# Kernel tuning notes

Hardware: AMD Instinct MI355X
Metric: run time of the kernel (lower is better)

The kernel has to match this reference:

```python
import jax, jax.numpy as jnp
import numpy as np

M = 8      # num_modules
H = 128    # hidden_size per module
IN = 512   # input_size
MH = M * H

def _block_mask():
    # mask[mi*H:(mi+1)*H, mi*H:] = 1 (module mi reads modules >= mi)
    m = np.zeros((MH, MH), dtype=np.float32)
    for mi in range(M):
        m[mi*H:(mi+1)*H, mi*H:] = 1.0
    return jnp.asarray(m)

def _active_sizes(T):
    # number of active modules at step t: t=0 -> M, else min(M, trailing_zeros(t)+1)
    sizes = []
    for t in range(T):
        ma = 0
        while t % (2 ** ma) == 0 and ma < M:
            ma += 1
        sizes.append(ma * H)
    return jnp.asarray(np.array(sizes, dtype=np.int32))

def setup_inputs() -> dict:
    key = jax.random.key(0)
    k1, k2, k3, k4 = jax.random.split(key, 4)
    T, B = 256, 128
    scale = 1.0 / np.sqrt(MH)
    x = jax.random.normal(k1, (T, B, IN), dtype=jnp.float32)
    h_prev = jnp.zeros((B, MH), dtype=jnp.float32)
    Wxh = jax.random.normal(k2, (MH, IN), dtype=jnp.float32) * scale
    Whh = jax.random.normal(k3, (MH, MH), dtype=jnp.float32) * scale
    bh = jax.random.normal(k4, (MH,), dtype=jnp.float32) * scale
    return {"x": x, "h_prev": h_prev, "Wxh": Wxh, "Whh": Whh, "bh": bh}

def reference(x, h_prev, Wxh, Whh, bh):
    T = x.shape[0]
    mask = _block_mask()
    Whh_m = Whh * mask  # clockwork block-triangular mask, reapplied as in torch
    thresholds = _active_sizes(T)          # [T] active hidden width per step
    idx = jnp.arange(MH)

    # Precompute input projections for all timesteps: [T, B, MH]
    xW = jnp.einsum('tbi,hi->tbh', x, Wxh)

    def step(h, inp):
        xw_t, thr = inp
        # full-width update; rows < thr equal the torch sliced-matmul result
        h_full = h @ Whh_m.T + xw_t + bh
        h_new = jnp.where(idx < thr, h_full, h)
        return h_new, h_new

    h_last, out = jax.lax.scan(step, h_prev, (xW, thresholds))
    return (out, h_last)
```

## Files before the change

kernel.cpp:

```cpp
#include <hip/hip_runtime.h>
#include <hip/hip_bf16.h>


#define TT 256
#define BB 128
#define INW 512
#define HH 128
#define MHW 1024

typedef __bf16 bf16x8 __attribute__((ext_vector_type(8)));
typedef __bf16 bf16x4 __attribute__((ext_vector_type(4)));
typedef float f32x4 __attribute__((ext_vector_type(4)));

__constant__ unsigned int c_hmod_off[8] = {
    0u, 4194304u, 6291456u, 7340032u, 7864320u, 8126464u, 8257536u, 8323072u};

__device__ __forceinline__ int active_thr(int t) {
    int ma = (t == 0) ? 8 : min(__ffs(t), 8);
    return ma * HH;
}

__device__ __forceinline__ unsigned short f2bf(float f) {
    union { float f; unsigned int u; } v{f};
    unsigned int r = v.u + 0x7FFFu + ((v.u >> 16) & 1u);
    return (unsigned short)(r >> 16);
}
__device__ __forceinline__ unsigned int pack2(float lo, float hi) {
    return (unsigned int)f2bf(lo) | ((unsigned int)f2bf(hi) << 16);
}
__device__ __forceinline__ float bf2f(unsigned short u) {
    union { unsigned int i; float f; } v;
    v.i = ((unsigned int)u) << 16;
    return v.f;
}

__device__ __forceinline__ void gld_lds16(const float* g, char* l) {
    __builtin_amdgcn_global_load_lds(
        (const __attribute__((address_space(1))) void*)g,
        (__attribute__((address_space(3))) void*)l, 16, 0, 0);
}

#define TILE_B 16384

__device__ __forceinline__ void stage_load(float4 (&v)[8],
                                           const float* __restrict__ src,
                                           int stride, int tid) {
    int k4 = (tid & 15) * 4;
    int r0 = tid >> 4;
#pragma unroll
    for (int p = 0; p < 8; ++p)
        v[p] = *reinterpret_cast<const float4*>(src + (size_t)(p * 16 + r0) * stride + k4);
}

__device__ __forceinline__ void stage_write(char* dst, const float4 (&v)[8], int tid) {
    int k8 = (tid & 15) * 8;
    int r0 = tid >> 4;
#pragma unroll
    for (int p = 0; p < 8; ++p) {
        int row = p * 16 + r0;
        ushort4 b;
        b.x = f2bf(v[p].x); b.y = f2bf(v[p].y);
        b.z = f2bf(v[p].z); b.w = f2bf(v[p].w);
        int off = (row * 128 + k8) ^ ((row & 7) << 4);
        *reinterpret_cast<ushort4*>(dst + off) = b;
    }
}

__device__ __forceinline__ void stage_load_h16(uint4 (&v)[4],
                                               const unsigned short* __restrict__ src,
                                               int tid) {
    int k16 = (tid & 7) * 8;
    int r0 = tid >> 3;
#pragma unroll
    for (int p = 0; p < 4; ++p)
        v[p] = *reinterpret_cast<const uint4*>(src + (size_t)(p * 32 + r0) * HH + k16);
}
__device__ __forceinline__ void stage_write_h16(char* dst, const uint4 (&v)[4], int tid) {
    int k16 = (tid & 7) * 8;
    int r0 = tid >> 3;
#pragma unroll
    for (int p = 0; p < 4; ++p) {
        int row = p * 32 + r0;
        int off = (row * 128 + k16 * 2) ^ ((row & 7) << 4);
        *reinterpret_cast<uint4*>(dst + off) = v[p];
    }
}

__device__ __forceinline__ bf16x8 frag_ld(const char* tile, int row, int ks, int lane) {
    int off = (row * 128 + ks * 64 + (lane >> 4) * 16) ^ ((row & 7) << 4);
    return *reinterpret_cast<const bf16x8*>(tile + off);
}

__device__ __forceinline__ bf16x8 frag_ld_f32(const char* tile, int row, int ks, int g) {
    int off = ((row << 8) + ks * 128 + g * 32) ^ ((row & 7) << 4);
    f32x4 a = *reinterpret_cast<const f32x4*>(tile + off);
    f32x4 b = *reinterpret_cast<const f32x4*>(tile + (off ^ 16));
    bf16x8 u;
    u[0] = (__bf16)a[0]; u[1] = (__bf16)a[1]; u[2] = (__bf16)a[2]; u[3] = (__bf16)a[3];
    u[4] = (__bf16)b[0]; u[5] = (__bf16)b[1]; u[6] = (__bf16)b[2]; u[7] = (__bf16)b[3];
    return u;
}

__device__ __forceinline__ void mfma_tile(const char* sA, const char* sB,
                                          f32x4 (&acc)[4][4], int lane,
                                          int wr, int wc) {
#pragma unroll
    for (int ks = 0; ks < 2; ++ks) {
        bf16x8 fa[4], fb[4];
#pragma unroll
        for (int i = 0; i < 4; ++i) {
            fa[i] = frag_ld(sA, wr + i * 16 + (lane & 15), ks, lane);
            fb[i] = frag_ld(sB, wc + i * 16 + (lane & 15), ks, lane);
        }
#pragma unroll
        for (int i = 0; i < 4; ++i)
#pragma unroll
            for (int j = 0; j < 4; ++j)
                acc[i][j] = __builtin_amdgcn_mfma_f32_16x16x32_bf16(
                    fa[i], fb[j], acc[i][j], 0, 0, 0);
    }
}

__global__ __launch_bounds__(256) void k_xw(const float* __restrict__ x,
                                            const float* __restrict__ Wxh,
                                            const float* __restrict__ bh,
                                            float* __restrict__ xwb) {
    __shared__ char ldsW[2][32768];
    __shared__ char ldsX[2][16384];
    int id = blockIdx.x >> 1, half = blockIdx.x & 1;
    int rt = 0, rem = id;
    while (rem >= (256 >> rt)) { rem -= 256 >> rt; ++rt; }
    int t = rem << rt;

    int tid = threadIdx.x, lane = tid & 63, wid = tid >> 6;
    int l15 = lane & 15, g = lane >> 4;
    int wr = (wid >> 1) * 64, wc = (wid & 1) * 32;

    const float* gW[8];
    const float* gX[4];
    {
        int kb = (lane & 15) * 16;
#pragma unroll
        for (int i = 0; i < 8; ++i) {
            int row = i * 16 + wid * 4 + (lane >> 4);
            int kf = (kb ^ ((row & 7) << 4)) >> 2;
            gW[i] = Wxh + (size_t)(rt * 128 + row) * INW + kf;
        }
#pragma unroll
        for (int i = 0; i < 4; ++i) {
            int row = i * 16 + wid * 4 + (lane >> 4);
            int kf = (kb ^ ((row & 7) << 4)) >> 2;
            gX[i] = x + ((size_t)t * BB + half * 64 + row) * INW + kf;
        }
    }
#pragma unroll
    for (int i = 0; i < 8; ++i)
        gld_lds16(gW[i], &ldsW[0][0] + i * 4096 + wid * 1024);
#pragma unroll
    for (int i = 0; i < 4; ++i)
        gld_lds16(gX[i], &ldsX[0][0] + i * 4096 + wid * 1024);

    f32x4 acc[4][2] = {};
    for (int c = 0; c < 8; ++c) {
        int cur = c & 1;
        __syncthreads();
        if (c < 7) {
#pragma unroll
            for (int i = 0; i < 8; ++i)
                gld_lds16(gW[i] + (c + 1) * 64,
                          &ldsW[cur ^ 1][0] + i * 4096 + wid * 1024);
#pragma unroll
            for (int i = 0; i < 4; ++i)
                gld_lds16(gX[i] + (c + 1) * 64,
                          &ldsX[cur ^ 1][0] + i * 4096 + wid * 1024);
        }
#pragma unroll
        for (int ks = 0; ks < 2; ++ks) {
            bf16x8 fa[4], fb[2];
#pragma unroll
            for (int i = 0; i < 4; ++i)
                fa[i] = frag_ld_f32(&ldsW[cur][0], wr + i * 16 + l15, ks, g);
#pragma unroll
            for (int j = 0; j < 2; ++j)
                fb[j] = frag_ld_f32(&ldsX[cur][0], wc + j * 16 + l15, ks, g);
#pragma unroll
            for (int i = 0; i < 4; ++i)
#pragma unroll
                for (int j = 0; j < 2; ++j)
                    acc[i][j] = __builtin_amdgcn_mfma_f32_16x16x32_bf16(
                        fa[i], fb[j], acc[i][j], 0, 0, 0);
        }
    }
#pragma unroll
    for (int i = 0; i < 4; ++i) {
        int rbase = rt * 128 + wr + i * 16 + g * 4;
        float4 bias = *reinterpret_cast<const float4*>(&bh[rbase]);
#pragma unroll
        for (int j = 0; j < 2; ++j) {
            int b = half * 64 + wc + j * 16 + l15;
            float4 v = make_float4(acc[i][j][0] + bias.x, acc[i][j][1] + bias.y,
                                   acc[i][j][2] + bias.z, acc[i][j][3] + bias.w);
            *reinterpret_cast<float4*>(
                &xwb[(size_t)(t * BB + b) * MHW + rbase]) = v;
        }
    }
}

__global__ __launch_bounds__(256) void k_u(const float* __restrict__ Whh,
                                           const float* __restrict__ hprev,
                                           const unsigned short* __restrict__ hmod,
                                           float* __restrict__ xwb, int mi) {
    int k = blockIdx.x;
    int t = k << mi;
    __shared__ char lds[4 * TILE_B];
    int tid = threadIdx.x, lane = tid & 63, wid = tid >> 6;
    int wr = (wid >> 1) * 64, wc = (wid & 1) * 64;

    int ntile = 2 * (7 - mi);
    f32x4 acc[4][4] = {};

    if (k == 0) {
        auto srcs = [&](int tt, const float*& pa, const float*& ph) {
            int j = mi + 1 + (tt >> 1);
            int c0 = (tt & 1) * 64;
            pa = Whh + (size_t)(mi * HH) * MHW + j * HH + c0;
            ph = hprev + j * HH + c0;
        };
        float4 vA[8], vH[8];
        const float *pa, *ph;
        srcs(0, pa, ph);
        stage_load(vA, pa, MHW, tid);
        stage_load(vH, ph, MHW, tid);
        stage_write(lds, vA, tid);
        stage_write(lds + TILE_B, vH, tid);
        for (int tt = 0; tt < ntile; ++tt) {
            int cur = tt & 1;
            __syncthreads();
            if (tt + 1 < ntile) {
                srcs(tt + 1, pa, ph);
                stage_load(vA, pa, MHW, tid);
                stage_load(vH, ph, MHW, tid);
            }
            mfma_tile(lds + cur * 2 * TILE_B, lds + cur * 2 * TILE_B + TILE_B,
                      acc, lane, wr, wc);
            if (tt + 1 < ntile) {
                stage_write(lds + (cur ^ 1) * 2 * TILE_B, vA, tid);
                stage_write(lds + (cur ^ 1) * 2 * TILE_B + TILE_B, vH, tid);
            }
        }
    } else {
        auto srcs = [&](int tt, const float*& pa, const unsigned short*& ph) {
            int j = mi + 1 + (tt >> 1);
            int c0 = (tt & 1) * 64;
            pa = Whh + (size_t)(mi * HH) * MHW + j * HH + c0;
            int g = (t - 1) >> j;
            ph = hmod + c_hmod_off[j] + (size_t)g * BB * HH + c0;
        };
        float4 vA[8];
        uint4 vH[4];
        const float* pa;
        const unsigned short* ph;
        srcs(0, pa, ph);
        stage_load(vA, pa, MHW, tid);
        stage_load_h16(vH, ph, tid);
        stage_write(lds, vA, tid);
        stage_write_h16(lds + TILE_B, vH, tid);
        for (int tt = 0; tt < ntile; ++tt) {
            int cur = tt & 1;
            __syncthreads();
            if (tt + 1 < ntile) {
                srcs(tt + 1, pa, ph);
                stage_load(vA, pa, MHW, tid);
                stage_load_h16(vH, ph, tid);
            }
            mfma_tile(lds + cur * 2 * TILE_B, lds + cur * 2 * TILE_B + TILE_B,
                      acc, lane, wr, wc);
            if (tt + 1 < ntile) {
                stage_write(lds + (cur ^ 1) * 2 * TILE_B, vA, tid);
                stage_write_h16(lds + (cur ^ 1) * 2 * TILE_B + TILE_B, vH, tid);
            }
        }
    }
#pragma unroll
    for (int i = 0; i < 4; ++i) {
        int rbase = wr + i * 16 + (lane >> 4) * 4;
#pragma unroll
        for (int j = 0; j < 4; ++j) {
            int b = wc + j * 16 + (lane & 15);
            float4* p = reinterpret_cast<float4*>(
                &xwb[(size_t)(t * BB + b) * MHW + mi * HH + rbase]);
            float4 v = *p;
            v.x += acc[i][j][0]; v.y += acc[i][j][1];
            v.z += acc[i][j][2]; v.w += acc[i][j][3];
            *p = v;
        }
    }
}

#define SYNC_LDS()                                              \
    do {                                                        \
        asm volatile("s_waitcnt lgkmcnt(0)" ::: "memory");      \
        __builtin_amdgcn_sched_barrier(0);                      \
        __builtin_amdgcn_s_barrier();                           \
        __builtin_amdgcn_sched_barrier(0);                      \
    } while (0)
#define SYNC_VM24()                                             \
    do {                                                        \
        asm volatile("s_waitcnt vmcnt(24)" ::: "memory");       \
        __builtin_amdgcn_sched_barrier(0);                      \
        __builtin_amdgcn_s_barrier();                           \
        __builtin_amdgcn_sched_barrier(0);                      \
    } while (0)

__global__ __launch_bounds__(256) void k_phase(const float* __restrict__ Whh,
                                               const float* __restrict__ hprev,
                                               const float* __restrict__ xwb,
                                               unsigned short* __restrict__ hmod,
                                               int mi) {
    int b0 = blockIdx.x * 16;
    int tid = threadIdx.x, lane = tid & 63, wid = tid >> 6;
    int l15 = lane & 15, g = lane >> 4;
    __shared__ char sH[2][4096];
    __shared__ char sU[8][8192];
    int Tm = TT >> mi;

    if (wid < 2) {
        bf16x8 Af[4][4];
        {
            const float* Ab = Whh + (size_t)(mi * HH) * MHW + mi * HH;
#pragma unroll
            for (int mm = 0; mm < 4; ++mm) {
                const float* row = Ab + (size_t)(64 * wid + mm * 16 + l15) * MHW;
#pragma unroll
                for (int kf = 0; kf < 4; ++kf) {
                    float4 v0 = *reinterpret_cast<const float4*>(row + kf * 32 + g * 8);
                    float4 v1 = *reinterpret_cast<const float4*>(row + kf * 32 + g * 8 + 4);
                    bf16x8 u;
                    u[0] = (__bf16)v0.x; u[1] = (__bf16)v0.y;
                    u[2] = (__bf16)v0.z; u[3] = (__bf16)v0.w;
                    u[4] = (__bf16)v1.x; u[5] = (__bf16)v1.y;
                    u[6] = (__bf16)v1.z; u[7] = (__bf16)v1.w;
                    Af[mm][kf] = u;
                }
            }
        }
#pragma unroll
        for (int p = 0; p < 2; ++p) {
            int tt = tid + p * 128;
            int b = tt >> 4, r8 = (tt & 15) * 8;
            const float* hp = hprev + (size_t)(b0 + b) * MHW + mi * HH + r8;
            float4 v0 = *reinterpret_cast<const float4*>(hp);
            float4 v1 = *reinterpret_cast<const float4*>(hp + 4);
            uint4 pk;
            pk.x = pack2(v0.x, v0.y); pk.y = pack2(v0.z, v0.w);
            pk.z = pack2(v1.x, v1.y); pk.w = pack2(v1.z, v1.w);
            int off = (b * 256 + r8 * 2) ^ ((b & 7) << 4);
            *reinterpret_cast<uint4*>(&sH[0][0] + off) = pk;
        }
        int roff[4], woff[4], uoff[4];
#pragma unroll
        for (int kf = 0; kf < 4; ++kf)
            roff[kf] = (l15 * 256 + kf * 64 + g * 16) ^ ((l15 & 7) << 4);
#pragma unroll
        for (int mm = 0; mm < 4; ++mm) {
            woff[mm] = (l15 * 256 + (64 * wid + mm * 16 + g * 4) * 2) ^ ((l15 & 7) << 4);
            uoff[mm] = (16 * wid + 4 * mm + g) * 256 + l15 * 16;
        }
        SYNC_LDS();

        for (int K = 0; K < Tm; ++K) {
            int cur = K & 1;
            const char* ub = &sU[K & 7][0];
            f32x4 acc[4], acc2[4];
#pragma unroll
            for (int mm = 0; mm < 4; ++mm) {
                acc[mm] = *reinterpret_cast<const f32x4*>(ub + uoff[mm]);
                acc2[mm] = (f32x4){0.f, 0.f, 0.f, 0.f};
            }
            bf16x8 Bf[4];
#pragma unroll
            for (int kf = 0; kf < 4; ++kf)
                Bf[kf] = *reinterpret_cast<const bf16x8*>(&sH[cur][0] + roff[kf]);
#pragma unroll
            for (int mm = 0; mm < 4; ++mm) {
                acc[mm] = __builtin_amdgcn_mfma_f32_16x16x32_bf16(
                    Af[mm][0], Bf[0], acc[mm], 0, 0, 0);
                acc2[mm] = __builtin_amdgcn_mfma_f32_16x16x32_bf16(
                    Af[mm][2], Bf[2], acc2[mm], 0, 0, 0);
                acc[mm] = __builtin_amdgcn_mfma_f32_16x16x32_bf16(
                    Af[mm][1], Bf[1], acc[mm], 0, 0, 0);
                acc2[mm] = __builtin_amdgcn_mfma_f32_16x16x32_bf16(
                    Af[mm][3], Bf[3], acc2[mm], 0, 0, 0);
            }
#pragma unroll
            for (int mm = 0; mm < 4; ++mm) {
                acc[mm] += acc2[mm];
                bf16x4 pk;
                pk[0] = (__bf16)acc[mm][0]; pk[1] = (__bf16)acc[mm][1];
                pk[2] = (__bf16)acc[mm][2]; pk[3] = (__bf16)acc[mm][3];
                *reinterpret_cast<bf16x4*>(&sH[cur ^ 1][0] + woff[mm]) = pk;
            }
            SYNC_LDS();
        }
    } else if (wid == 2) {
        const float* ubase = xwb + (size_t)(b0 + l15) * MHW + mi * HH + g * 4;
#pragma unroll
        for (int q = 0; q < 4; ++q) {
            int t = min(q, Tm - 1) << mi;
            const float* pt = ubase + (size_t)t * BB * MHW;
#pragma unroll
            for (int p = 0; p < 8; ++p)
                gld_lds16(pt + p * 16, &sU[q][0] + p * 1024);
        }
        SYNC_VM24();
        for (int K = 0; K < Tm; ++K) {
            int t = min(K + 4, Tm - 1) << mi;
            int slot = (K + 4) & 7;
            const float* pt = ubase + (size_t)t * BB * MHW;
#pragma unroll
            for (int p = 0; p < 8; ++p)
                gld_lds16(pt + p * 16, &sU[slot][0] + p * 1024);
            SYNC_VM24();
        }
        asm volatile("s_waitcnt vmcnt(0)" ::: "memory");
    } else {
        int bq = lane >> 2;
        int rr = (lane & 3) * 32;
        unsigned short* hm =
            hmod + c_hmod_off[mi] + (size_t)(b0 + bq) * HH + rr;
        int soff[4];
#pragma unroll
        for (int c = 0; c < 4; ++c)
            soff[c] = (bq * 256 + (rr + c * 8) * 2) ^ ((bq & 7) << 4);
        SYNC_LDS();
        for (int K = 0; K < Tm; ++K) {
            if (K >= 1) {
                uint4 h[4];
#pragma unroll
                for (int c = 0; c < 4; ++c)
                    h[c] = *reinterpret_cast<const uint4*>(&sH[K & 1][0] + soff[c]);
                unsigned short* dst = hm + (size_t)(K - 1) * BB * HH;
#pragma unroll
                for (int c = 0; c < 4; ++c)
                    *reinterpret_cast<uint4*>(dst + c * 8) = h[c];
            }
            SYNC_LDS();
        }
        {
            uint4 h[4];
#pragma unroll
            for (int c = 0; c < 4; ++c)
                h[c] = *reinterpret_cast<const uint4*>(&sH[Tm & 1][0] + soff[c]);
            unsigned short* dst = hm + (size_t)(Tm - 1) * BB * HH;
#pragma unroll
            for (int c = 0; c < 4; ++c)
                *reinterpret_cast<uint4*>(dst + c * 8) = h[c];
        }
    }
}

__global__ __launch_bounds__(256) void k_out(const unsigned short* __restrict__ hmod,
                                             float* __restrict__ out) {
    int b = blockIdx.x, t = blockIdx.y;
    int tid = threadIdx.x;
    int i = tid * 4;
    int j = i >> 7;
    int k = t >> j;
    ushort4 h = *reinterpret_cast<const ushort4*>(
        &hmod[c_hmod_off[j] + ((size_t)k * BB + b) * HH + (i & 127)]);
    float4 v = make_float4(bf2f(h.x), bf2f(h.y), bf2f(h.z), bf2f(h.w));
    *reinterpret_cast<float4*>(&out[((size_t)t * BB + b) * MHW + i]) = v;
    if (t == TT - 1) {
        *reinterpret_cast<float4*>(
            &out[(size_t)TT * BB * MHW + (size_t)b * MHW + i]) = v;
    }
}

extern "C" void kernel_launch(void* const* d_in, const int* in_sizes, int n_in,
                              void* d_out, int out_size, void* d_ws, size_t ws_size,
                              hipStream_t stream) {
    const float* x = (const float*)d_in[0];
    const float* hprev = (const float*)d_in[1];
    const float* Wxh = (const float*)d_in[2];
    const float* Whh = (const float*)d_in[3];
    const float* bh = (const float*)d_in[4];
    float* out = (float*)d_out;

    float* xwb = out;
    unsigned short* hmod = (unsigned short*)d_ws;

    k_xw<<<dim3(1020), 256, 0, stream>>>(x, Wxh, bh, xwb);

    for (int mi = 7; mi >= 0; --mi) {
        if (mi < 7)
            k_u<<<dim3(TT >> mi), 256, 0, stream>>>(Whh, hprev, hmod, xwb, mi);
        k_phase<<<8, 256, 0, stream>>>(Whh, hprev, xwb, hmod, mi);
    }

    k_out<<<dim3(128, 256), 256, 0, stream>>>(hmod, out);
}
```

Baseline: 469.7 us.

## Halve sequential recurrence steps by squaring the diagonal block (A^2 doubling)

Precomputes A^2 for each module's diagonal recurrence block and a combined input term v = A·u_even + u_odd, so the serial phase kernel advances two timesteps per iteration and only produces odd-indexed states. A parallel k_even kernel then fills in the even-indexed states from the preceding odd state. This halves the length of the latency-bound sequential chain, at the cost of two extra parallel kernels per module and extra bf16 rounding through the squared matrix.

```diff
diff --git a/kernel.cpp b/kernel.cpp
--- a/kernel.cpp
+++ b/kernel.cpp
@@ -202,6 +202,52 @@
                                    acc[i][j][2] + bias.z, acc[i][j][3] + bias.w);
             *reinterpret_cast<float4*>(
                 &xwb[(size_t)(t * BB + b) * MHW + rbase]) = v;
+        }
+    }
+}
+
+__global__ __launch_bounds__(256) void k_a2(const float* __restrict__ Whh,
+                                            float* __restrict__ a2) {
+    int mi = blockIdx.x;
+    __shared__ char lds[2 * TILE_B];
+    int tid = threadIdx.x, lane = tid & 63, wid = tid >> 6;
+    int l15 = lane & 15, g = lane >> 4;
+    int wr = (wid >> 1) * 64, wc = (wid & 1) * 64;
+    const float* Ab = Whh + (size_t)(mi * HH) * MHW + mi * HH;
+    f32x4 acc[4][4] = {};
+    for (int c0 = 0; c0 < 128; c0 += 64) {
+        float4 vA[8];
+        stage_load(vA, Ab + c0, MHW, tid);
+        __syncthreads();
+        stage_write(lds, vA, tid);
+        {
+            int k4 = (tid & 15) * 4;
+            int r0 = tid >> 4;
+#pragma unroll
+            for (int p = 0; p < 8; ++p) {
+                int row = p * 16 + r0;
+                ushort4 b;
+                b.x = f2bf(Ab[(size_t)(c0 + k4 + 0) * MHW + row]);
+                b.y = f2bf(Ab[(size_t)(c0 + k4 + 1) * MHW + row]);
+                b.z = f2bf(Ab[(size_t)(c0 + k4 + 2) * MHW + row]);
+                b.w = f2bf(Ab[(size_t)(c0 + k4 + 3) * MHW + row]);
+                int off = (row * 128 + k4 * 2) ^ ((row & 7) << 4);
+                *reinterpret_cast<ushort4*>(lds + TILE_B + off) = b;
+            }
+        }
+        __syncthreads();
+        mfma_tile(lds, lds + TILE_B, acc, lane, wr, wc);
+    }
+    float* dst = a2 + mi * 16384;
+#pragma unroll
+    for (int i = 0; i < 4; ++i) {
+        int r0 = wr + i * 16 + g * 4;
+#pragma unroll
+        for (int jq = 0; jq < 4; ++jq) {
+            int c = wc + jq * 16 + l15;
+#pragma unroll
+            for (int rr = 0; rr < 4; ++rr)
+                dst[(size_t)(r0 + rr) * 128 + c] = acc[i][jq][rr];
         }
     }
 }
@@ -297,6 +343,130 @@
     }
 }
 
+__global__ __launch_bounds__(256) void k_v(const float* __restrict__ Whh,
+                                           const float* __restrict__ xwb,
+                                           float* __restrict__ vbuf, int mi) {
+    int j = blockIdx.x;
+    int t0 = (2 * j) << mi, t1 = (2 * j + 1) << mi;
+    __shared__ char lds[4 * TILE_B];
+    int tid = threadIdx.x, lane = tid & 63, wid = tid >> 6;
+    int l15 = lane & 15, g = lane >> 4;
+    int wr = (wid >> 1) * 64, wc = (wid & 1) * 64;
+
+    const float* Ab = Whh + (size_t)(mi * HH) * MHW + mi * HH;
+    const float* Hb = xwb + (size_t)t0 * BB * MHW + mi * HH;
+    float4 vA[8], vH[8];
+    stage_load(vA, Ab, MHW, tid);
+    stage_load(vH, Hb, MHW, tid);
+    stage_write(lds, vA, tid);
+    stage_write(lds + TILE_B, vH, tid);
+    f32x4 acc[4][4] = {};
+    for (int tt = 0; tt < 2; ++tt) {
+        int cur = tt & 1;
+        __syncthreads();
+        if (tt == 0) {
+            stage_load(vA, Ab + 64, MHW, tid);
+            stage_load(vH, Hb + 64, MHW, tid);
+        }
+        mfma_tile(lds + cur * 2 * TILE_B, lds + cur * 2 * TILE_B + TILE_B,
+                  acc, lane, wr, wc);
+        if (tt == 0) {
+            stage_write(lds + 2 * TILE_B, vA, tid);
+            stage_write(lds + 3 * TILE_B, vH, tid);
+        }
+    }
+#pragma unroll
+    for (int i = 0; i < 4; ++i) {
+        int rbase = wr + i * 16 + g * 4;
+#pragma unroll
+        for (int jq = 0; jq < 4; ++jq) {
+            int b = wc + jq * 16 + l15;
+            float4 u1 = *reinterpret_cast<const float4*>(
+                &xwb[(size_t)(t1 * BB + b) * MHW + mi * HH + rbase]);
+            float4 v = make_float4(acc[i][jq][0] + u1.x, acc[i][jq][1] + u1.y,
+                                   acc[i][jq][2] + u1.z, acc[i][jq][3] + u1.w);
+            *reinterpret_cast<float4*>(
+                &vbuf[((size_t)j * BB + b) * HH + rbase]) = v;
+        }
+    }
+}
+
+__global__ __launch_bounds__(256) void k_even(const float* __restrict__ Whh,
+                                              const float* __restrict__ hprev,
+                                              const float* __restrict__ xwb,
+                                              unsigned short* __restrict__ hmod,
+                                              int mi) {
+    int j = blockIdx.x;
+    int t0 = (2 * j) << mi;
+    __shared__ char lds[4 * TILE_B];
+    int tid = threadIdx.x, lane = tid & 63, wid = tid >> 6;
+    int l15 = lane & 15, g = lane >> 4;
+    int wr = (wid >> 1) * 64, wc = (wid & 1) * 64;
+
+    const float* Ab = Whh + (size_t)(mi * HH) * MHW + mi * HH;
+    f32x4 acc[4][4] = {};
+    if (j == 0) {
+        const float* Hb = hprev + mi * HH;
+        float4 vA[8], vH[8];
+        stage_load(vA, Ab, MHW, tid);
+        stage_load(vH, Hb, MHW, tid);
+        stage_write(lds, vA, tid);
+        stage_write(lds + TILE_B, vH, tid);
+        for (int tt = 0; tt < 2; ++tt) {
+            int cur = tt & 1;
+            __syncthreads();
+            if (tt == 0) {
+                stage_load(vA, Ab + 64, MHW, tid);
+                stage_load(vH, Hb + 64, MHW, tid);
+            }
+            mfma_tile(lds + cur * 2 * TILE_B, lds + cur * 2 * TILE_B + TILE_B,
+                      acc, lane, wr, wc);
+            if (tt == 0) {
+                stage_write(lds + 2 * TILE_B, vA, tid);
+                stage_write(lds + 3 * TILE_B, vH, tid);
+            }
+        }
+    } else {
+        const unsigned short* Hb =
+            hmod + c_hmod_off[mi] + (size_t)(2 * j - 1) * BB * HH;
+        float4 vA[8];
+        uint4 vH[4];
+        stage_load(vA, Ab, MHW, tid);
+        stage_load_h16(vH, Hb, tid);
+        stage_write(lds, vA, tid);
+        stage_write_h16(lds + TILE_B, vH, tid);
+        for (int tt = 0; tt < 2; ++tt) {
+            int cur = tt & 1;
+            __syncthreads();
+            if (tt == 0) {
+                stage_load(vA, Ab + 64, MHW, tid);
+                stage_load_h16(vH, Hb + 64, tid);
+            }
+            mfma_tile(lds + cur * 2 * TILE_B, lds + cur * 2 * TILE_B + TILE_B,
+                      acc, lane, wr, wc);
+            if (tt == 0) {
+                stage_write(lds + 2 * TILE_B, vA, tid);
+                stage_write_h16(lds + 3 * TILE_B, vH, tid);
+            }
+        }
+    }
+#pragma unroll
+    for (int i = 0; i < 4; ++i) {
+        int rbase = wr + i * 16 + g * 4;
+#pragma unroll
+        for (int jq = 0; jq < 4; ++jq) {
+            int b = wc + jq * 16 + l15;
+            float4 u0 = *reinterpret_cast<const float4*>(
+                &xwb[(size_t)(t0 * BB + b) * MHW + mi * HH + rbase]);
+            uint2 pk;
+            pk.x = pack2(acc[i][jq][0] + u0.x, acc[i][jq][1] + u0.y);
+            pk.y = pack2(acc[i][jq][2] + u0.z, acc[i][jq][3] + u0.w);
+            *reinterpret_cast<uint2*>(
+                &hmod[c_hmod_off[mi] + ((size_t)(2 * j) * BB + b) * HH + rbase]) = pk;
+        }
+    }
+}
+
 #define SYNC_LDS()                                              \
     do {                                                        \
         asm volatile("s_waitcnt lgkmcnt(0)" ::: "memory");      \
@@ -312,9 +482,9 @@
         __builtin_amdgcn_sched_barrier(0);                      \
     } while (0)
 
-__global__ __launch_bounds__(256) void k_phase(const float* __restrict__ Whh,
+__global__ __launch_bounds__(256) void k_phase(const float* __restrict__ a2,
                                                const float* __restrict__ hprev,
-                                               const float* __restrict__ xwb,
+                                               const float* __restrict__ vbuf,
                                                unsigned short* __restrict__ hmod,
                                                int mi) {
     int b0 = blockIdx.x * 16;
@@ -322,15 +492,15 @@
     int l15 = lane & 15, g = lane >> 4;
     __shared__ char sH[2][4096];
     __shared__ char sU[8][8192];
-    int Tm = TT >> mi;
+    int Tm_s = 128 >> mi;
 
     if (wid < 2) {
         bf16x8 Af[4][4];
         {
-            const float* Ab = Whh + (size_t)(mi * HH) * MHW + mi * HH;
+            const float* Ab = a2 + mi * 16384;
 #pragma unroll
             for (int mm = 0; mm < 4; ++mm) {
-                const float* row = Ab + (size_t)(64 * wid + mm * 16 + l15) * MHW;
+                const float* row = Ab + (size_t)(64 * wid + mm * 16 + l15) * 128;
 #pragma unroll
                 for (int kf = 0; kf < 4; ++kf) {
                     float4 v0 = *reinterpret_cast<const float4*>(row + kf * 32 + g * 8);
@@ -368,7 +538,7 @@
         }
         SYNC_LDS();
 
-        for (int K = 0; K < Tm; ++K) {
+        for (int K = 0; K < Tm_s; ++K) {
             int cur = K & 1;
             const char* ub = &sU[K & 7][0];
             f32x4 acc[4], acc2[4];
@@ -403,20 +573,20 @@
             SYNC_LDS();
         }
     } else if (wid == 2) {
-        const float* ubase = xwb + (size_t)(b0 + l15) * MHW + mi * HH + g * 4;
+        const float* ubase = vbuf + (size_t)(b0 + l15) * HH + g * 4;
 #pragma unroll
         for (int q = 0; q < 4; ++q) {
-            int t = min(q, Tm - 1) << mi;
-            const float* pt = ubase + (size_t)t * BB * MHW;
+            int jj = min(q, Tm_s - 1);
+            const float* pt = ubase + (size_t)jj * BB * HH;
 #pragma unroll
             for (int p = 0; p < 8; ++p)
                 gld_lds16(pt + p * 16, &sU[q][0] + p * 1024);
         }
         SYNC_VM24();
-        for (int K = 0; K < Tm; ++K) {
-            int t = min(K + 4, Tm - 1) << mi;
+        for (int K = 0; K < Tm_s; ++K) {
+            int jj = min(K + 4, Tm_s - 1);
             int slot = (K + 4) & 7;
-            const float* pt = ubase + (size_t)t * BB * MHW;
+            const float* pt = ubase + (size_t)jj * BB * HH;
 #pragma unroll
             for (int p = 0; p < 8; ++p)
                 gld_lds16(pt + p * 16, &sU[slot][0] + p * 1024);
@@ -433,13 +603,13 @@
         for (int c = 0; c < 4; ++c)
             soff[c] = (bq * 256 + (rr + c * 8) * 2) ^ ((bq & 7) << 4);
         SYNC_LDS();
-        for (int K = 0; K < Tm; ++K) {
+        for (int K = 0; K < Tm_s; ++K) {
             if (K >= 1) {
                 uint4 h[4];
 #pragma unroll
                 for (int c = 0; c < 4; ++c)
                     h[c] = *reinterpret_cast<const uint4*>(&sH[K & 1][0] + soff[c]);
-                unsigned short* dst = hm + (size_t)(K - 1) * BB * HH;
+                unsigned short* dst = hm + (size_t)(2 * K - 1) * BB * HH;
 #pragma unroll
                 for (int c = 0; c < 4; ++c)
                     *reinterpret_cast<uint4*>(dst + c * 8) = h[c];
@@ -450,8 +620,8 @@
             uint4 h[4];
 #pragma unroll
             for (int c = 0; c < 4; ++c)
-                h[c] = *reinterpret_cast<const uint4*>(&sH[Tm & 1][0] + soff[c]);
-            unsigned short* dst = hm + (size_t)(Tm - 1) * BB * HH;
+                h[c] = *reinterpret_cast<const uint4*>(&sH[Tm_s & 1][0] + soff[c]);
+            unsigned short* dst = hm + (size_t)(2 * Tm_s - 1) * BB * HH;
 #pragma unroll
             for (int c = 0; c < 4; ++c)
                 *reinterpret_cast<uint4*>(dst + c * 8) = h[c];
@@ -488,13 +658,18 @@
 
     float* xwb = out;
     unsigned short* hmod = (unsigned short*)d_ws;
+    float* vbuf = (float*)((char*)d_ws + 16711680);
+    float* a2 = (float*)((char*)d_ws + 16711680 + 8388608);
 
     k_xw<<<dim3(1020), 256, 0, stream>>>(x, Wxh, bh, xwb);
+    k_a2<<<dim3(8), 256, 0, stream>>>(Whh, a2);
 
     for (int mi = 7; mi >= 0; --mi) {
         if (mi < 7)
             k_u<<<dim3(TT >> mi), 256, 0, stream>>>(Whh, hprev, hmod, xwb, mi);
-        k_phase<<<8, 256, 0, stream>>>(Whh, hprev, xwb, hmod, mi);
+        k_v<<<dim3(128 >> mi), 256, 0, stream>>>(Whh, xwb, vbuf, mi);
+        k_phase<<<8, 256, 0, stream>>>(a2, hprev, vbuf, hmod, mi);
+        k_even<<<dim3(128 >> mi), 256, 0, stream>>>(Whh, hprev, xwb, hmod, mi);
     }
 
     k_out<<<dim3(128, 256), 256, 0, stream>>>(hmod, out);
```

After: 511.7 us. 1.09x slower.

## Split recurrence into odd/even chains using squared diagonal block A^2

Applied to the files above, without the earlier changes.

Precomputes the squared diagonal recurrence block A^2 per module in a new kernel. The phase kernel then runs two independent half-length chains, odd and even steps, on separate warps, so h_{k+2} = A^2 h_k + A u_{k+1} + u_{k+2}. This roughly halves the serial dependency length of the sequential scan and doubles the warps and U prefetch buffers in flight. In exchange each step does twice the MFMA work, uses more registers and LDS, and adds extra bf16 rounding through A^2 and the converted u fragments.

```diff
diff --git a/kernel.cpp b/kernel.cpp
--- a/kernel.cpp
+++ b/kernel.cpp
@@ -202,6 +202,52 @@
                                    acc[i][j][2] + bias.z, acc[i][j][3] + bias.w);
             *reinterpret_cast<float4*>(
                 &xwb[(size_t)(t * BB + b) * MHW + rbase]) = v;
+        }
+    }
+}
+
+__global__ __launch_bounds__(256) void k_a2(const float* __restrict__ Whh,
+                                            float* __restrict__ a2) {
+    int mi = blockIdx.x;
+    __shared__ char lds[2 * TILE_B];
+    int tid = threadIdx.x, lane = tid & 63, wid = tid >> 6;
+    int l15 = lane & 15, g = lane >> 4;
+    int wr = (wid >> 1) * 64, wc = (wid & 1) * 64;
+    const float* Ab = Whh + (size_t)(mi * HH) * MHW + mi * HH;
+    f32x4 acc[4][4] = {};
+    for (int c0 = 0; c0 < 128; c0 += 64) {
+        float4 vA[8];
+        stage_load(vA, Ab + c0, MHW, tid);
+        __syncthreads();
+        stage_write(lds, vA, tid);
+        {
+            int k4 = (tid & 15) * 4;
+            int r0 = tid >> 4;
+#pragma unroll
+            for (int p = 0; p < 8; ++p) {
+                int row = p * 16 + r0;
+                ushort4 b;
+                b.x = f2bf(Ab[(size_t)(c0 + k4 + 0) * MHW + row]);
+                b.y = f2bf(Ab[(size_t)(c0 + k4 + 1) * MHW + row]);
+                b.z = f2bf(Ab[(size_t)(c0 + k4 + 2) * MHW + row]);
+                b.w = f2bf(Ab[(size_t)(c0 + k4 + 3) * MHW + row]);
+                int off = (row * 128 + k4 * 2) ^ ((row & 7) << 4);
+                *reinterpret_cast<ushort4*>(lds + TILE_B + off) = b;
+            }
+        }
+        __syncthreads();
+        mfma_tile(lds, lds + TILE_B, acc, lane, wr, wc);
+    }
+    float* dst = a2 + mi * 16384;
+#pragma unroll
+    for (int i = 0; i < 4; ++i) {
+        int r0 = wr + i * 16 + g * 4;
+#pragma unroll
+        for (int jq = 0; jq < 4; ++jq) {
+            int c = wc + jq * 16 + l15;
+#pragma unroll
+            for (int rr = 0; rr < 4; ++rr)
+                dst[(size_t)(r0 + rr) * 128 + c] = acc[i][jq][rr];
         }
     }
 }
@@ -304,15 +350,16 @@
         __builtin_amdgcn_s_barrier();                           \
         __builtin_amdgcn_sched_barrier(0);                      \
     } while (0)
-#define SYNC_VM24()                                             \
+#define SYNC_VM(NS)                                             \
     do {                                                        \
-        asm volatile("s_waitcnt vmcnt(24)" ::: "memory");       \
+        asm volatile("s_waitcnt vmcnt(" NS ")" ::: "memory");   \
         __builtin_amdgcn_sched_barrier(0);                      \
         __builtin_amdgcn_s_barrier();                           \
         __builtin_amdgcn_sched_barrier(0);                      \
     } while (0)
 
-__global__ __launch_bounds__(256) void k_phase(const float* __restrict__ Whh,
+__global__ __launch_bounds__(512) void k_phase(const float* __restrict__ a2,
+                                               const float* __restrict__ Whh,
                                                const float* __restrict__ hprev,
                                                const float* __restrict__ xwb,
                                                unsigned short* __restrict__ hmod,
@@ -320,77 +367,160 @@
     int b0 = blockIdx.x * 16;
     int tid = threadIdx.x, lane = tid & 63, wid = tid >> 6;
     int l15 = lane & 15, g = lane >> 4;
-    __shared__ char sH[2][4096];
-    __shared__ char sU[8][8192];
-    int Tm = TT >> mi;
-
-    if (wid < 2) {
-        bf16x8 Af[4][4];
+    __shared__ char sHo[2][4096];
+    __shared__ char sHe[2][4096];
+    __shared__ char sU[16][8192];
+    int Tm = TT >> mi, Tm2 = Tm >> 1;
+
+    if (wid < 4) {
+        int w = wid & 1;
+        bool is_odd = wid < 2;
+        char(*sH)[4096] = is_odd ? sHo : sHe;
+
+        bf16x8 A2f[4][4], A1f[4][4];
         {
-            const float* Ab = Whh + (size_t)(mi * HH) * MHW + mi * HH;
+            const float* Ab2 = a2 + mi * 16384;
+            const float* Ab1 = Whh + (size_t)(mi * HH) * MHW + mi * HH;
 #pragma unroll
             for (int mm = 0; mm < 4; ++mm) {
-                const float* row = Ab + (size_t)(64 * wid + mm * 16 + l15) * MHW;
+                const float* r2 = Ab2 + (size_t)(64 * w + mm * 16 + l15) * 128;
+                const float* r1 = Ab1 + (size_t)(64 * w + mm * 16 + l15) * MHW;
 #pragma unroll
                 for (int kf = 0; kf < 4; ++kf) {
-                    float4 v0 = *reinterpret_cast<const float4*>(row + kf * 32 + g * 8);
-                    float4 v1 = *reinterpret_cast<const float4*>(row + kf * 32 + g * 8 + 4);
-                    bf16x8 u;
-                    u[0] = (__bf16)v0.x; u[1] = (__bf16)v0.y;
-                    u[2] = (__bf16)v0.z; u[3] = (__bf16)v0.w;
-                    u[4] = (__bf16)v1.x; u[5] = (__bf16)v1.y;
-                    u[6] = (__bf16)v1.z; u[7] = (__bf16)v1.w;
-                    Af[mm][kf] = u;
+                    float4 a0 = *reinterpret_cast<const float4*>(r2 + kf * 32 + g * 8);
+                    float4 a1 = *reinterpret_cast<const float4*>(r2 + kf * 32 + g * 8 + 4);
+                    float4 b0v = *reinterpret_cast<const float4*>(r1 + kf * 32 + g * 8);
+                    float4 b1v = *reinterpret_cast<const float4*>(r1 + kf * 32 + g * 8 + 4);
+                    bf16x8 u2, u1;
+                    u2[0] = (__bf16)a0.x; u2[1] = (__bf16)a0.y;
+                    u2[2] = (__bf16)a0.z; u2[3] = (__bf16)a0.w;
+                    u2[4] = (__bf16)a1.x; u2[5] = (__bf16)a1.y;
+                    u2[6] = (__bf16)a1.z; u2[7] = (__bf16)a1.w;
+                    u1[0] = (__bf16)b0v.x; u1[1] = (__bf16)b0v.y;
+                    u1[2] = (__bf16)b0v.z; u1[3] = (__bf16)b0v.w;
+                    u1[4] = (__bf16)b1v.x; u1[5] = (__bf16)b1v.y;
+                    u1[6] = (__bf16)b1v.z; u1[7] = (__bf16)b1v.w;
+                    A2f[mm][kf] = u2;
+                    A1f[mm][kf] = u1;
                 }
             }
         }
-#pragma unroll
-        for (int p = 0; p < 2; ++p) {
-            int tt = tid + p * 128;
-            int b = tt >> 4, r8 = (tt & 15) * 8;
-            const float* hp = hprev + (size_t)(b0 + b) * MHW + mi * HH + r8;
-            float4 v0 = *reinterpret_cast<const float4*>(hp);
-            float4 v1 = *reinterpret_cast<const float4*>(hp + 4);
-            uint4 pk;
-            pk.x = pack2(v0.x, v0.y); pk.y = pack2(v0.z, v0.w);
-            pk.z = pack2(v1.x, v1.y); pk.w = pack2(v1.z, v1.w);
-            int off = (b * 256 + r8 * 2) ^ ((b & 7) << 4);
-            *reinterpret_cast<uint4*>(&sH[0][0] + off) = pk;
-        }
-        int roff[4], woff[4], uoff[4];
-#pragma unroll
-        for (int kf = 0; kf < 4; ++kf)
+        bf16x8 hpf[4];
+        if (is_odd) {
+#pragma unroll
+            for (int p = 0; p < 2; ++p) {
+                int tt = tid + p * 128;
+                int b = tt >> 4, r8 = (tt & 15) * 8;
+                const float* hp = hprev + (size_t)(b0 + b) * MHW + mi * HH + r8;
+                float4 v0 = *reinterpret_cast<const float4*>(hp);
+                float4 v1 = *reinterpret_cast<const float4*>(hp + 4);
+                uint4 pk;
+                pk.x = pack2(v0.x, v0.y); pk.y = pack2(v0.z, v0.w);
+                pk.z = pack2(v1.x, v1.y); pk.w = pack2(v1.z, v1.w);
+                int off = (b * 256 + r8 * 2) ^ ((b & 7) << 4);
+                *reinterpret_cast<uint4*>(&sHo[0][0] + off) = pk;
+            }
+        } else {
+            const float* hp = hprev + (size_t)(b0 + l15) * MHW + mi * HH;
+#pragma unroll
+            for (int kf = 0; kf < 4; ++kf) {
+                float4 v0 = *reinterpret_cast<const float4*>(hp + kf * 32 + g * 8);
+                float4 v1 = *reinterpret_cast<const float4*>(hp + kf * 32 + g * 8 + 4);
+                bf16x8 u;
+                u[0] = (__bf16)v0.x; u[1] = (__bf16)v0.y;
+                u[2] = (__bf16)v0.z; u[3] = (__bf16)v0.w;
+                u[4] = (__bf16)v1.x; u[5] = (__bf16)v1.y;
+                u[6] = (__bf16)v1.z; u[7] = (__bf16)v1.w;
+                hpf[kf] = u;
+            }
+        }
+        int roff[4], woff[4], uoff[4], buoff[4];
+#pragma unroll
+        for (int kf = 0; kf < 4; ++kf) {
             roff[kf] = (l15 * 256 + kf * 64 + g * 16) ^ ((l15 & 7) << 4);
+            buoff[kf] = (kf * 8 + g * 2) * 256 + l15 * 16;
+        }
 #pragma unroll
         for (int mm = 0; mm < 4; ++mm) {
-            woff[mm] = (l15 * 256 + (64 * wid + mm * 16 + g * 4) * 2) ^ ((l15 & 7) << 4);
-            uoff[mm] = (16 * wid + 4 * mm + g) * 256 + l15 * 16;
+            woff[mm] = (l15 * 256 + (64 * w + mm * 16 + g * 4) * 2) ^ ((l15 & 7) << 4);
+            uoff[mm] = (16 * w + 4 * mm + g) * 256 + l15 * 16;
         }
         SYNC_LDS();
 
-        for (int K = 0; K < Tm; ++K) {
-            int cur = K & 1;
-            const char* ub = &sU[K & 7][0];
+        int K0 = 0;
+        if (!is_odd) {
+            const char* ubS = &sU[0][0];
             f32x4 acc[4], acc2[4];
 #pragma unroll
             for (int mm = 0; mm < 4; ++mm) {
-                acc[mm] = *reinterpret_cast<const f32x4*>(ub + uoff[mm]);
+                acc[mm] = *reinterpret_cast<const f32x4*>(ubS + uoff[mm]);
                 acc2[mm] = (f32x4){0.f, 0.f, 0.f, 0.f};
             }
-            bf16x8 Bf[4];
-#pragma unroll
-            for (int kf = 0; kf < 4; ++kf)
-                Bf[kf] = *reinterpret_cast<const bf16x8*>(&sH[cur][0] + roff[kf]);
 #pragma unroll
             for (int mm = 0; mm < 4; ++mm) {
                 acc[mm] = __builtin_amdgcn_mfma_f32_16x16x32_bf16(
-                    Af[mm][0], Bf[0], acc[mm], 0, 0, 0);
+                    A1f[mm][0], hpf[0], acc[mm], 0, 0, 0);
                 acc2[mm] = __builtin_amdgcn_mfma_f32_16x16x32_bf16(
-                    Af[mm][2], Bf[2], acc2[mm], 0, 0, 0);
+                    A1f[mm][2], hpf[2], acc2[mm], 0, 0, 0);
                 acc[mm] = __builtin_amdgcn_mfma_f32_16x16x32_bf16(
-                    Af[mm][1], Bf[1], acc[mm], 0, 0, 0);
+                    A1f[mm][1], hpf[1], acc[mm], 0, 0, 0);
                 acc2[mm] = __builtin_amdgcn_mfma_f32_16x16x32_bf16(
-                    Af[mm][3], Bf[3], acc2[mm], 0, 0, 0);
+                    A1f[mm][3], hpf[3], acc2[mm], 0, 0, 0);
+            }
+#pragma unroll
+            for (int mm = 0; mm < 4; ++mm) {
+                acc[mm] += acc2[mm];
+                bf16x4 pk;
+                pk[0] = (__bf16)acc[mm][0]; pk[1] = (__bf16)acc[mm][1];
+                pk[2] = (__bf16)acc[mm][2]; pk[3] = (__bf16)acc[mm][3];
+                *reinterpret_cast<bf16x4*>(&sHe[1][0] + woff[mm]) = pk;
+            }
+            SYNC_LDS();
+            K0 = 1;
+        }
+        for (int K = K0; K < Tm2; ++K) {
+            int cur = K & 1;
+            int seed_idx = is_odd ? (2 * K + 1) : (2 * K);
+            int frag_idx = is_odd ? (2 * K) : (2 * K - 1);
+            const char* ubS = &sU[seed_idx & 15][0];
+            const char* ubF = &sU[frag_idx & 15][0];
+            f32x4 acc[4], acc2[4];
+#pragma unroll
+            for (int mm = 0; mm < 4; ++mm) {
+                acc[mm] = *reinterpret_cast<const f32x4*>(ubS + uoff[mm]);
+                acc2[mm] = (f32x4){0.f, 0.f, 0.f, 0.f};
+            }
+            bf16x8 Bh[4], Bu[4];
+#pragma unroll
+            for (int kf = 0; kf < 4; ++kf) {
+                Bh[kf] = *reinterpret_cast<const bf16x8*>(&sH[cur][0] + roff[kf]);
+                f32x4 ua = *reinterpret_cast<const f32x4*>(ubF + buoff[kf]);
+                f32x4 ub = *reinterpret_cast<const f32x4*>(ubF + buoff[kf] + 256);
+                bf16x8 u;
+                u[0] = (__bf16)ua[0]; u[1] = (__bf16)ua[1];
+                u[2] = (__bf16)ua[2]; u[3] = (__bf16)ua[3];
+                u[4] = (__bf16)ub[0]; u[5] = (__bf16)ub[1];
+                u[6] = (__bf16)ub[2]; u[7] = (__bf16)ub[3];
+                Bu[kf] = u;
+            }
+#pragma unroll
+            for (int mm = 0; mm < 4; ++mm) {
+                acc[mm] = __builtin_amdgcn_mfma_f32_16x16x32_bf16(
+                    A2f[mm][0], Bh[0], acc[mm], 0, 0, 0);
+                acc2[mm] = __builtin_amdgcn_mfma_f32_16x16x32_bf16(
+                    A2f[mm][2], Bh[2], acc2[mm], 0, 0, 0);
+                acc[mm] = __builtin_amdgcn_mfma_f32_16x16x32_bf16(
+                    A2f[mm][1], Bh[1], acc[mm], 0, 0, 0);
+                acc2[mm] = __builtin_amdgcn_mfma_f32_16x16x32_bf16(
+                    A2f[mm][3], Bh[3], acc2[mm], 0, 0, 0);
+                acc[mm] = __builtin_amdgcn_mfma_f32_16x16x32_bf16(
+                    A1f[mm][0], Bu[0], acc[mm], 0, 0, 0);
+                acc2[mm] = __builtin_amdgcn_mfma_f32_16x16x32_bf16(
+                    A1f[mm][2], Bu[2], acc2[mm], 0, 0, 0);
+                acc[mm] = __builtin_amdgcn_mfma_f32_16x16x32_bf16(
+                    A1f[mm][1], Bu[1], acc[mm], 0, 0, 0);
+                acc2[mm] = __builtin_amdgcn_mfma_f32_16x16x32_bf16(
+                    A1f[mm][3], Bu[3], acc2[mm], 0, 0, 0);
             }
 #pragma unroll
             for (int mm = 0; mm < 4; ++mm) {
@@ -402,44 +532,51 @@
             }
             SYNC_LDS();
         }
-    } else if (wid == 2) {
+    } else if (wid == 4 || wid == 7) {
         const float* ubase = xwb + (size_t)(b0 + l15) * MHW + mi * HH + g * 4;
-#pragma unroll
-        for (int q = 0; q < 4; ++q) {
-            int t = min(q, Tm - 1) << mi;
-            const float* pt = ubase + (size_t)t * BB * MHW;
+        auto fill = [&](int k) {
+            int kk = min(k, Tm - 1);
+            const float* pt = ubase + ((size_t)(kk << mi)) * BB * MHW;
+            char* dst = &sU[kk & 15][0];
 #pragma unroll
             for (int p = 0; p < 8; ++p)
-                gld_lds16(pt + p * 16, &sU[q][0] + p * 1024);
-        }
-        SYNC_VM24();
-        for (int K = 0; K < Tm; ++K) {
-            int t = min(K + 4, Tm - 1) << mi;
-            int slot = (K + 4) & 7;
-            const float* pt = ubase + (size_t)t * BB * MHW;
-#pragma unroll
-            for (int p = 0; p < 8; ++p)
-                gld_lds16(pt + p * 16, &sU[slot][0] + p * 1024);
-            SYNC_VM24();
+                gld_lds16(pt + p * 16, dst + p * 1024);
+        };
+        if (wid == 4) {
+            fill(0); fill(2); fill(4); fill(6); fill(8); fill(10);
+            SYNC_VM("40");
+            for (int K = 0; K < Tm2; ++K) {
+                fill(2 * K + 12);
+                SYNC_VM("40");
+            }
+        } else {
+            fill(1); fill(3); fill(5); fill(7); fill(9);
+            SYNC_VM("32");
+            for (int K = 0; K < Tm2; ++K) {
+                fill(2 * K + 11);
+                SYNC_VM("32");
+            }
         }
         asm volatile("s_waitcnt vmcnt(0)" ::: "memory");
     } else {
+        bool so = (wid == 5);
+        const char(*sH)[4096] = so ? sHo : sHe;
         int bq = lane >> 2;
         int rr = (lane & 3) * 32;
-        unsigned short* hm =
-            hmod + c_hmod_off[mi] + (size_t)(b0 + bq) * HH + rr;
+        unsigned short* hm = hmod + c_hmod_off[mi] + (size_t)(b0 + bq) * HH + rr;
         int soff[4];
 #pragma unroll
         for (int c = 0; c < 4; ++c)
             soff[c] = (bq * 256 + (rr + c * 8) * 2) ^ ((bq & 7) << 4);
         SYNC_LDS();
-        for (int K = 0; K < Tm; ++K) {
+        for (int K = 0; K < Tm2; ++K) {
             if (K >= 1) {
                 uint4 h[4];
 #pragma unroll
                 for (int c = 0; c < 4; ++c)
                     h[c] = *reinterpret_cast<const uint4*>(&sH[K & 1][0] + soff[c]);
-                unsigned short* dst = hm + (size_t)(K - 1) * BB * HH;
+                int slot = so ? (2 * K - 1) : (2 * K - 2);
+                unsigned short* dst = hm + (size_t)slot * BB * HH;
 #pragma unroll
                 for (int c = 0; c < 4; ++c)
                     *reinterpret_cast<uint4*>(dst + c * 8) = h[c];
@@ -450,8 +587,9 @@
             uint4 h[4];
 #pragma unroll
             for (int c = 0; c < 4; ++c)
-                h[c] = *reinterpret_cast<const uint4*>(&sH[Tm & 1][0] + soff[c]);
-            unsigned short* dst = hm + (size_t)(Tm - 1) * BB * HH;
+                h[c] = *reinterpret_cast<const uint4*>(&sH[Tm2 & 1][0] + soff[c]);
+            int slot = so ? (2 * Tm2 - 1) : (2 * Tm2 - 2);
+            unsigned short* dst = hm + (size_t)slot * BB * HH;
 #pragma unroll
             for (int c = 0; c < 4; ++c)
                 *reinterpret_cast<uint4*>(dst + c * 8) = h[c];
@@ -488,13 +626,15 @@
 
     float* xwb = out;
     unsigned short* hmod = (unsigned short*)d_ws;
+    float* a2 = (float*)((char*)d_ws + 16711680);
 
     k_xw<<<dim3(1020), 256, 0, stream>>>(x, Wxh, bh, xwb);
+    k_a2<<<dim3(8), 256, 0, stream>>>(Whh, a2);
 
     for (int mi = 7; mi >= 0; --mi) {
         if (mi < 7)
             k_u<<<dim3(TT >> mi), 256, 0, stream>>>(Whh, hprev, hmod, xwb, mi);
-        k_phase<<<8, 256, 0, stream>>>(Whh, hprev, xwb, hmod, mi);
+        k_phase<<<8, 512, 0, stream>>>(a2, Whh, hprev, xwb, hmod, mi);
     }
 
     k_out<<<dim3(128, 256), 256, 0, stream>>>(hmod, out);
```

Result: slower. 590.4 us (+25.7%).
